# Kernel optimization log

Hardware: AMD Instinct MI355X
Metric: run time of the kernel (lower is better)

Reference implementation:

```python
import jax, jax.numpy as jnp
import numpy as np

N = 40000   # nodes
E = 600000  # edges
F = 128     # feature_size
H = 128     # hidden_channels
G = 32      # graphs in batch
C = 6       # classes


def setup_inputs() -> dict:
    key = jax.random.key(0)
    ks = jax.random.split(key, 20)
    x = jax.random.normal(ks[0], (N, F), jnp.float32)
    edge_index = jax.random.randint(ks[1], (2, E), 0, N, jnp.int32)
    batch = jnp.sort(jax.random.randint(ks[2], (N,), 0, G, jnp.int32))

    def lin_w(k, fan_in, fan_out):
        return jax.random.uniform(k, (fan_in, fan_out), jnp.float32,
                                  -1.0, 1.0) / np.sqrt(fan_in)

    inp = {"x": x, "edge_index": edge_index, "batch": batch,
           # GraphConv1: feature_size -> hidden (root + rel weights, bias)
           "w1_root": lin_w(ks[3], F, H), "w1_rel": lin_w(ks[4], F, H),
           "b1": jnp.zeros((H,), jnp.float32),
           # GraphConv2: hidden -> hidden
           "w2_root": lin_w(ks[5], H, H), "w2_rel": lin_w(ks[6], H, H),
           "b2": jnp.zeros((H,), jnp.float32),
           # GCNConv 3..5
           "w3": lin_w(ks[7], H, H), "b3": jnp.zeros((H,), jnp.float32),
           "w4": lin_w(ks[8], H, H), "b4": jnp.zeros((H,), jnp.float32),
           "w5": lin_w(ks[9], H, H), "b5": jnp.zeros((H,), jnp.float32),
           # final Linear(hidden, 6)
           "lin_w": lin_w(ks[10], H, C), "lin_b": jnp.zeros((C,), jnp.float32)}
    return inp


def _graph_conv(x, w_root, w_rel, b, src, dst, n):
    # PyG GraphConv (aggr='add'): out_i = W_root x_i + W_rel * sum_{j->i} x_j + b
    agg = jax.ops.segment_sum(x[src], dst, num_segments=n)
    return agg @ w_rel + x @ w_root + b


def _gcn_conv(x, w, b, src_sl, dst_sl, deg_inv_sqrt, n):
    # PyG GCNConv: out = D^-1/2 (A+I) D^-1/2 (X W) + b
    h = x @ w
    norm = deg_inv_sqrt[src_sl] * deg_inv_sqrt[dst_sl]  # [E+N]
    out = jax.ops.segment_sum(h[src_sl] * norm[:, None], dst_sl, num_segments=n)
    return out + b


def reference(x, edge_index, batch, w1_root, w1_rel, b1, w2_root, w2_rel, b2,
              w3, b3, w4, b4, w5, b5, lin_w, lin_b):
    src, dst = edge_index[0], edge_index[1]
    # self-loops for GCN layers
    loop = jnp.arange(N, dtype=edge_index.dtype)
    src_sl = jnp.concatenate([src, loop])
    dst_sl = jnp.concatenate([dst, loop])
    deg = jax.ops.segment_sum(jnp.ones((E + N,), x.dtype), dst_sl, num_segments=N)
    deg_inv_sqrt = jax.lax.rsqrt(deg)  # deg >= 1 due to self-loops

    h = jax.nn.relu(_graph_conv(x, w1_root, w1_rel, b1, src, dst, N))
    h = jax.nn.relu(_graph_conv(h, w2_root, w2_rel, b2, src, dst, N))
    h = jax.nn.relu(_gcn_conv(h, w3, b3, src_sl, dst_sl, deg_inv_sqrt, N))
    h = jax.nn.relu(_gcn_conv(h, w4, b4, src_sl, dst_sl, deg_inv_sqrt, N))
    h = _gcn_conv(h, w5, b5, src_sl, dst_sl, deg_inv_sqrt, N)

    # global_mean_pool over batch assignment
    counts = jax.ops.segment_sum(jnp.ones((N,), h.dtype), batch, num_segments=G)
    sums = jax.ops.segment_sum(h, batch, num_segments=G)
    embedding = sums / jnp.maximum(counts, 1.0)[:, None]  # [G, H]

    # dropout p=0.5 is identity in eval mode
    logits = embedding @ lin_w + lin_b  # [G, C]
    return (logits, embedding)
```

## Files before the change

kernel.cpp:

```cpp
#include <hip/hip_runtime.h>
#include <hip/hip_fp8.h>

#define Nn 40000
#define Ee 600000
#define Hh 128
#define Gg 32
#define Cc 6
#define CAP 64
#define NT (Nn / 16)
#define LSTR 136
#define PADW 0x9C409C40u

typedef __bf16 bf16x8 __attribute__((ext_vector_type(8)));
typedef float floatx4 __attribute__((ext_vector_type(4)));
typedef float floatx2 __attribute__((ext_vector_type(2)));
typedef unsigned short u16;
typedef unsigned int u32;
typedef unsigned char u8;

__device__ __forceinline__ u16 f2b(float f) {
    union { float f; u32 i; } v; v.f = f;
    u32 r = v.i + 0x7fffu + ((v.i >> 16) & 1u);
    return (u16)(r >> 16);
}
__device__ __forceinline__ u32 pack2(float a, float b) {
    return (u32)f2b(a) | ((u32)f2b(b) << 16);
}
__device__ __forceinline__ u8 f8e(float f) {
    __hip_fp8_e4m3 v(f); return (u8)v.__x;
}
__device__ __forceinline__ u8 f8e_hw(float f) {
    return (u8)(__builtin_amdgcn_cvt_pk_fp8_f32(f, f, 0, false) & 0xff);
}

__global__ __launch_bounds__(256) void k_setup(int* cursor, float* emb,
                                               u16* xb, u16* hA16, u8* xf8, u8* hA8, u8* hB8,
                                               float* dinv, u16* colidx,
                                               const float* __restrict__ x,
                                               const float* w0, const float* w1, const float* w2,
                                               const float* w3, const float* w4, const float* w5,
                                               const float* w6, u16* __restrict__ pwdst) {
    int gid = blockIdx.x * 256 + threadIdx.x;
    if (gid < Nn) cursor[gid] = 0;
    if (gid < Gg * Hh) emb[gid] = 0.f;
    if (blockIdx.x == 0) {
        int t = threadIdx.x;
        uint4 z = { 0, 0, 0, 0 };
        if (t < 16)              *(uint4*)(xb  + (size_t)Nn * 128 + t * 8) = z;
        else if (t < 32)         *(uint4*)(hA16 + (size_t)Nn * 128 + (t - 16) * 8) = z;
        else if (t < 40)         *(uint4*)(xf8 + (size_t)Nn * 128 + (t - 32) * 16) = z;
        else if (t < 48)         *(uint4*)(hA8 + (size_t)Nn * 128 + (t - 40) * 16) = z;
        else if (t < 56)         *(uint4*)(hB8 + (size_t)Nn * 128 + (t - 48) * 16) = z;
        else if (t == 56)        dinv[Nn] = 0.f;
    }
    if (blockIdx.x < 448) {
        int idx = gid;
        if (idx < 7 * 16384) {
            const float* ws[7] = { w0, w1, w2, w3, w4, w5, w6 };
            int mat = idx >> 14, r = idx & 16383;
            int j = r & 7, n = (r >> 3) & 15, q = (r >> 7) & 3, nt = (r >> 9) & 7, t = r >> 12;
            pwdst[idx] = f2b(ws[mat][(t * 32 + q * 8 + j) * 128 + nt * 16 + n]);
        }
    } else {
        int gid2 = (blockIdx.x - 448) * 256 + threadIdx.x;
        int i = gid2 * 4;
        float4 v = *(const float4*)(x + i);
        ushort4 o = { f2b(v.x), f2b(v.y), f2b(v.z), f2b(v.w) };
        *(ushort4*)(xb + i) = o;
        u32 p8 = (u32)f8e(v.x) | ((u32)f8e(v.y) << 8) | ((u32)f8e(v.z) << 16) | ((u32)f8e(v.w) << 24);
        *(u32*)(xf8 + i) = p8;
        *(u32*)(colidx + gid2 * 2) = PADW;
    }
}

__global__ __launch_bounds__(256) void k_scatter(const int* __restrict__ src, const int* __restrict__ dst,
                                                 int* __restrict__ cursor, u16* __restrict__ colidx) {
    int i = blockIdx.x * 256 + threadIdx.x;
    if (i < Ee) {
        int d = dst[i];
        int p = atomicAdd(&cursor[d], 1);
        if (p < CAP) colidx[d * CAP + p] = (u16)src[i];
    }
}

#define UPC_ADD(V) { floatx2 p_;                                                          \
    p_ = __builtin_amdgcn_cvt_pk_f32_fp8((int)(V).x, false); a0 += p_.x; a1 += p_.y;      \
    p_ = __builtin_amdgcn_cvt_pk_f32_fp8((int)(V).x, true);  a2 += p_.x; a3 += p_.y;      \
    p_ = __builtin_amdgcn_cvt_pk_f32_fp8((int)(V).y, false); a4 += p_.x; a5 += p_.y;      \
    p_ = __builtin_amdgcn_cvt_pk_f32_fp8((int)(V).y, true);  a6 += p_.x; a7 += p_.y; }

#define UPC_FMA(V, d) { floatx2 p_;                                                                 \
    p_ = __builtin_amdgcn_cvt_pk_f32_fp8((int)(V).x, false); a0 += (d) * p_.x; a1 += (d) * p_.y;    \
    p_ = __builtin_amdgcn_cvt_pk_f32_fp8((int)(V).x, true);  a2 += (d) * p_.x; a3 += (d) * p_.y;    \
    p_ = __builtin_amdgcn_cvt_pk_f32_fp8((int)(V).y, false); a4 += (d) * p_.x; a5 += (d) * p_.y;    \
    p_ = __builtin_amdgcn_cvt_pk_f32_fp8((int)(V).y, true);  a6 += (d) * p_.x; a7 += (d) * p_.y; }

__global__ __launch_bounds__(256) void k_layer(const u8* __restrict__ hin8,
                                               const u16* __restrict__ hin16,
                                               const u16* __restrict__ Bp_agg,
                                               const u16* __restrict__ Bp_self,
                                               const float* __restrict__ bias,
                                               u16* __restrict__ hout16,
                                               u8* __restrict__ hout8,
                                               const int* __restrict__ cursor,
                                               const u16* __restrict__ pcol,
                                               float* __restrict__ dinv,
                                               const int* __restrict__ batch,
                                               float* __restrict__ emb,
                                               int gcn, int relu, int dopool, int wrdinv) {
    __shared__ u16 Asm[16 * LSTR];
    __shared__ float Psm[16][132];
    int wave = threadIdx.x >> 6, lane = threadIdx.x & 63;
    int m0 = blockIdx.x * 16;

    {
        int g = lane >> 4, l = lane & 15;
        int nloc = wave * 4 + g;
        int node = m0 + nloc;
        int c = cursor[node]; if (c > CAP) c = CAP;
        if (wrdinv && l == 0) dinv[node] = rsqrtf((float)(c + 1));
        int beg = node * CAP;
        int end = beg + ((c + 7) & ~7);
        float a0 = 0.f, a1 = 0.f, a2 = 0.f, a3 = 0.f, a4 = 0.f, a5 = 0.f, a6 = 0.f, a7 = 0.f;
        const u8* b8 = hin8 + l * 8;
        if (beg < end) {
            uint4 ip = *(const uint4*)(pcol + beg);
            if (gcn) {
                for (int e = beg; e < end; e += 8) {
                    int en = (e + 8 < end) ? (e + 8) : beg;
                    uint4 jp = *(const uint4*)(pcol + en);
                    u32 e0 = ip.x & 0xFFFFu, e1 = ip.x >> 16;
                    u32 e2 = ip.y & 0xFFFFu, e3 = ip.y >> 16;
                    u32 e4 = ip.z & 0xFFFFu, e5 = ip.z >> 16;
                    u32 e6 = ip.w & 0xFFFFu, e7 = ip.w >> 16;
                    float d0 = dinv[e0], d1 = dinv[e1], d2 = dinv[e2], d3 = dinv[e3];
                    float d4 = dinv[e4], d5 = dinv[e5], d6 = dinv[e6], d7 = dinv[e7];
                    uint2 v0 = *(const uint2*)(b8 + (size_t)e0 * 128);
                    uint2 v1 = *(const uint2*)(b8 + (size_t)e1 * 128);
                    uint2 v2 = *(const uint2*)(b8 + (size_t)e2 * 128);
                    uint2 v3 = *(const uint2*)(b8 + (size_t)e3 * 128);
                    uint2 v4 = *(const uint2*)(b8 + (size_t)e4 * 128);
                    uint2 v5 = *(const uint2*)(b8 + (size_t)e5 * 128);
                    uint2 v6 = *(const uint2*)(b8 + (size_t)e6 * 128);
                    uint2 v7 = *(const uint2*)(b8 + (size_t)e7 * 128);
                    UPC_FMA(v0, d0) UPC_FMA(v1, d1) UPC_FMA(v2, d2) UPC_FMA(v3, d3)
                    UPC_FMA(v4, d4) UPC_FMA(v5, d5) UPC_FMA(v6, d6) UPC_FMA(v7, d7)
                    ip = jp;
                }
            } else {
                for (int e = beg; e < end; e += 8) {
                    int en = (e + 8 < end) ? (e + 8) : beg;
                    uint4 jp = *(const uint4*)(pcol + en);
                    u32 e0 = ip.x & 0xFFFFu, e1 = ip.x >> 16;
                    u32 e2 = ip.y & 0xFFFFu, e3 = ip.y >> 16;
                    u32 e4 = ip.z & 0xFFFFu, e5 = ip.z >> 16;
                    u32 e6 = ip.w & 0xFFFFu, e7 = ip.w >> 16;
                    uint2 v0 = *(const uint2*)(b8 + (size_t)e0 * 128);
                    uint2 v1 = *(const uint2*)(b8 + (size_t)e1 * 128);
                    uint2 v2 = *(const uint2*)(b8 + (size_t)e2 * 128);
                    uint2 v3 = *(const uint2*)(b8 + (size_t)e3 * 128);
                    uint2 v4 = *(const uint2*)(b8 + (size_t)e4 * 128);
                    uint2 v5 = *(const uint2*)(b8 + (size_t)e5 * 128);
                    uint2 v6 = *(const uint2*)(b8 + (size_t)e6 * 128);
                    uint2 v7 = *(const uint2*)(b8 + (size_t)e7 * 128);
                    UPC_ADD(v0) UPC_ADD(v1) UPC_ADD(v2) UPC_ADD(v3)
                    UPC_ADD(v4) UPC_ADD(v5) UPC_ADD(v6) UPC_ADD(v7)
                    ip = jp;
                }
            }
        }
        if (gcn) {
            float di = dinv[node], d2n = di * di;
            uint2 us = *(const uint2*)(b8 + (size_t)node * 128);
            a0 *= di; a1 *= di; a2 *= di; a3 *= di;
            a4 *= di; a5 *= di; a6 *= di; a7 *= di;
            UPC_FMA(us, d2n)
        }
        uint4 o = { pack2(a0, a1), pack2(a2, a3), pack2(a4, a5), pack2(a6, a7) };
        *(uint4*)&Asm[nloc * LSTR + l * 8] = o;
    }
    __syncthreads();

    {
        int n = lane & 15, q = lane >> 4;
        floatx4 acc0 = (floatx4){0.f, 0.f, 0.f, 0.f};
        floatx4 acc1 = (floatx4){0.f, 0.f, 0.f, 0.f};
        int nt0 = wave * 2, nt1 = wave * 2 + 1;
#pragma unroll
        for (int t = 0; t < 4; t++) {
            bf16x8 a = *(const bf16x8*)&Asm[n * LSTR + q * 8 + t * 32];
            const u16* bp = Bp_agg + t * 4096 + q * 128 + n * 8;
            bf16x8 b0 = *(const bf16x8*)(bp + nt0 * 512);
            bf16x8 b1 = *(const bf16x8*)(bp + nt1 * 512);
            acc0 = __builtin_amdgcn_mfma_f32_16x16x32_bf16(a, b0, acc0, 0, 0, 0);
            acc1 = __builtin_amdgcn_mfma_f32_16x16x32_bf16(a, b1, acc1, 0, 0, 0);
        }
        if (!gcn) {
            const u16* arow = hin16 + (size_t)(m0 + n) * 128 + q * 8;
#pragma unroll
            for (int t = 0; t < 4; t++) {
                bf16x8 a = *(const bf16x8*)(arow + t * 32);
                const u16* bp = Bp_self + t * 4096 + q * 128 + n * 8;
                bf16x8 b0 = *(const bf16x8*)(bp + nt0 * 512);
                bf16x8 b1 = *(const bf16x8*)(bp + nt1 * 512);
                acc0 = __builtin_amdgcn_mfma_f32_16x16x32_bf16(a, b0, acc0, 0, 0, 0);
                acc1 = __builtin_amdgcn_mfma_f32_16x16x32_bf16(a, b1, acc1, 0, 0, 0);
            }
        }
        if (dopool) {
#pragma unroll
            for (int j = 0; j < 2; j++) {
                int col = (wave * 2 + j) * 16 + n;
                float bv = bias[col];
                floatx4 ac = j ? acc1 : acc0;
#pragma unroll
                for (int r = 0; r < 4; r++)
                    Psm[q * 4 + r][col] = ac[r] + bv;
            }
            __syncthreads();
            if (threadIdx.x < 128) {
                int col = threadIdx.x;
                int g0 = batch[m0], g1 = batch[m0 + 15];
                for (int g = g0; g <= g1; ++g) {
                    float s = 0.f;
#pragma unroll
                    for (int i = 0; i < 16; ++i)
                        if (batch[m0 + i] == g) s += Psm[i][col];
                    atomicAdd(&emb[g * 128 + col], s);
                }
            }
        } else {
#pragma unroll
            for (int j = 0; j < 2; j++) {
                int col = (wave * 2 + j) * 16 + n;
                float bv = bias[col];
                floatx4 ac = j ? acc1 : acc0;
#pragma unroll
                for (int r = 0; r < 4; r++) {
                    float v = ac[r] + bv;
                    if (relu) v = fmaxf(v, 0.f);
                    size_t idx = (size_t)(m0 + q * 4 + r) * 128 + col;
                    if (hout16) hout16[idx] = f2b(v);
                    if (hout8)  hout8[idx]  = f8e_hw(v);
                }
            }
        }
    }
}

__global__ __launch_bounds__(256) void k_final(const float* __restrict__ emb, const int* __restrict__ batch,
                                               const float* __restrict__ lw, const float* __restrict__ lb,
                                               float* __restrict__ out) {
    __shared__ float cnt[Gg];
    int t = threadIdx.x;
    if (t < Gg) {
        int lo = 0, hi = Nn;
        while (lo < hi) { int m = (lo + hi) >> 1; if (batch[m] < t) lo = m + 1; else hi = m; }
        int lb0 = lo;
        lo = 0; hi = Nn;
        int tg = t + 1;
        while (lo < hi) { int m = (lo + hi) >> 1; if (batch[m] < tg) lo = m + 1; else hi = m; }
        cnt[t] = fmaxf((float)(lo - lb0), 1.f);
    }
    __syncthreads();
    for (int i = t; i < Gg * Hh; i += 256) {
        int g = i >> 7;
        out[Gg * Cc + i] = emb[i] / cnt[g];
    }
    if (t < Gg * Cc) {
        int g = t / Cc, c = t % Cc;
        float cn = cnt[g];
        float s = lb[c];
        for (int f = 0; f < Hh; f++)
            s += (emb[g * 128 + f] / cn) * lw[f * Cc + c];
        out[t] = s;
    }
}

extern "C" void kernel_launch(void* const* d_in, const int* in_sizes, int n_in,
                              void* d_out, int out_size, void* d_ws, size_t ws_size,
                              hipStream_t stream) {
    const float* x       = (const float*)d_in[0];
    const int*   ei      = (const int*)d_in[1];
    const int*   batch   = (const int*)d_in[2];
    const float* w1_root = (const float*)d_in[3];
    const float* w1_rel  = (const float*)d_in[4];
    const float* b1      = (const float*)d_in[5];
    const float* w2_root = (const float*)d_in[6];
    const float* w2_rel  = (const float*)d_in[7];
    const float* b2      = (const float*)d_in[8];
    const float* w3      = (const float*)d_in[9];
    const float* b3      = (const float*)d_in[10];
    const float* w4      = (const float*)d_in[11];
    const float* b4      = (const float*)d_in[12];
    const float* w5      = (const float*)d_in[13];
    const float* b5      = (const float*)d_in[14];
    const float* lw      = (const float*)d_in[15];
    const float* lb      = (const float*)d_in[16];
    const int* srcp = ei;
    const int* dstp = ei + Ee;
    float* out = (float*)d_out;

    char* w = (char*)d_ws;
    size_t off = 0;
    auto alloc = [&](size_t bytes) { size_t r = off; off += (bytes + 255) & ~(size_t)255; return r; };
    int*   cursor  = (int*)(w + alloc(Nn * 4));
    u16*   colidx  = (u16*)(w + alloc((size_t)Nn * CAP * 2));
    float* dinv    = (float*)(w + alloc((Nn + 1) * 4));
    float* emb     = (float*)(w + alloc(Gg * Hh * 4));
    u16*   pw      = (u16*)(w + alloc(7 * 16384 * 2));
    u16*   xb      = (u16*)(w + alloc((size_t)(Nn + 1) * Hh * 2));
    u16*   hA16    = (u16*)(w + alloc((size_t)(Nn + 1) * Hh * 2));
    u8*    xf8     = (u8*)(w + alloc((size_t)(Nn + 1) * Hh));
    u8*    hA8     = (u8*)(w + alloc((size_t)(Nn + 1) * Hh));
    u8*    hB8     = (u8*)(w + alloc((size_t)(Nn + 1) * Hh));
    (void)ws_size;

    u16* pw1r = pw + 0 * 16384;
    u16* pw1l = pw + 1 * 16384;
    u16* pw2r = pw + 2 * 16384;
    u16* pw2l = pw + 3 * 16384;
    u16* pw3  = pw + 4 * 16384;
    u16* pw4  = pw + 5 * 16384;
    u16* pw5  = pw + 6 * 16384;
    const u16* nil16 = (const u16*)nullptr;
    u16* no16 = (u16*)nullptr;
    u8*  no8  = (u8*)nullptr;

    hipLaunchKernelGGL(k_setup, dim3(448 + Nn * Hh / 1024), dim3(256), 0, stream,
                       cursor, emb, xb, hA16, xf8, hA8, hB8, dinv, colidx,
                       x, w1_root, w1_rel, w2_root, w2_rel, w3, w4, w5, pw);
    hipLaunchKernelGGL(k_scatter, dim3((Ee + 255) / 256), dim3(256), 0, stream,
                       srcp, dstp, cursor, colidx);

    hipLaunchKernelGGL(k_layer, dim3(NT), dim3(256), 0, stream,
                       xf8, xb, pw1l, pw1r, b1, hA16, hA8, cursor, colidx, dinv, batch, emb, 0, 1, 0, 1);
    hipLaunchKernelGGL(k_layer, dim3(NT), dim3(256), 0, stream,
                       hA8, hA16, pw2l, pw2r, b2, no16, hB8, cursor, colidx, dinv, batch, emb, 0, 1, 0, 0);
    hipLaunchKernelGGL(k_layer, dim3(NT), dim3(256), 0, stream,
                       hB8, nil16, pw3, nil16, b3, no16, hA8, cursor, colidx, dinv, batch, emb, 1, 1, 0, 0);
    hipLaunchKernelGGL(k_layer, dim3(NT), dim3(256), 0, stream,
                       hA8, nil16, pw4, nil16, b4, no16, xf8, cursor, colidx, dinv, batch, emb, 1, 1, 0, 0);
    hipLaunchKernelGGL(k_layer, dim3(NT), dim3(256), 0, stream,
                       xf8, nil16, pw5, nil16, b5, no16, no8, cursor, colidx, dinv, batch, emb, 1, 0, 1, 0);

    hipLaunchKernelGGL(k_final, dim3(1), dim3(256), 0, stream, emb, batch, lw, lb, out);
}
```

Baseline: 252.7 us.

## Bin edges by destination range before scattering into CSR adjacency

Replaces the single random scatter of edges into per-node adjacency lists with two passes. The first pass buckets packed (src,dst) pairs into 16 destination-range bins using shared-memory counters. The second pass scatters each bin, with block classes mapped to bin subsets so the atomics and colidx writes of concurrent blocks stay within a narrower, more cache-local address range. This costs an extra kernel launch and an extra write and read of the edge buffer, and it relies on the 16-bit packing of src and dst indices.

```diff
diff --git a/kernel.cpp b/kernel.cpp
--- a/kernel.cpp
+++ b/kernel.cpp
@@ -10,6 +10,8 @@
 #define NT (Nn / 16)
 #define LSTR 136
 #define PADW 0x9C409C40u
+#define NBIN 16
+#define BINCAP 40960
 
 typedef __bf16 bf16x8 __attribute__((ext_vector_type(8)));
 typedef float floatx4 __attribute__((ext_vector_type(4)));
@@ -33,7 +35,7 @@
     return (u8)(__builtin_amdgcn_cvt_pk_fp8_f32(f, f, 0, false) & 0xff);
 }
 
-__global__ __launch_bounds__(256) void k_setup(int* cursor, float* emb,
+__global__ __launch_bounds__(256) void k_setup(int* cursor, float* emb, int* gbin,
                                                u16* xb, u16* hA16, u8* xf8, u8* hA8, u8* hB8,
                                                float* dinv, u16* colidx,
                                                const float* __restrict__ x,
@@ -43,6 +45,7 @@
     int gid = blockIdx.x * 256 + threadIdx.x;
     if (gid < Nn) cursor[gid] = 0;
     if (gid < Gg * Hh) emb[gid] = 0.f;
+    if (gid < NBIN) gbin[gid] = 0;
     if (blockIdx.x == 0) {
         int t = threadIdx.x;
         uint4 z = { 0, 0, 0, 0 };
@@ -73,13 +76,50 @@
     }
 }
 
-__global__ __launch_bounds__(256) void k_scatter(const int* __restrict__ src, const int* __restrict__ dst,
-                                                 int* __restrict__ cursor, u16* __restrict__ colidx) {
-    int i = blockIdx.x * 256 + threadIdx.x;
+__global__ __launch_bounds__(256) void k_bin(const int* __restrict__ src, const int* __restrict__ dst,
+                                             int* __restrict__ gbin, u32* __restrict__ ebuf,
+                                             int* __restrict__ cursor, u16* __restrict__ colidx) {
+    __shared__ int cnt[NBIN];
+    __shared__ int base[NBIN];
+    int tid = threadIdx.x;
+    int i = blockIdx.x * 256 + tid;
+    if (tid < NBIN) cnt[tid] = 0;
+    __syncthreads();
+    int bin = -1, myslot = 0, s = 0, d = 0;
     if (i < Ee) {
-        int d = dst[i];
-        int p = atomicAdd(&cursor[d], 1);
-        if (p < CAP) colidx[d * CAP + p] = (u16)src[i];
+        s = src[i];
+        d = dst[i];
+        bin = d / 2500;
+        myslot = atomicAdd(&cnt[bin], 1);
+    }
+    __syncthreads();
+    if (tid < NBIN) base[tid] = (cnt[tid] > 0) ? atomicAdd(&gbin[tid], cnt[tid]) : 0;
+    __syncthreads();
+    if (bin >= 0) {
+        int slot = base[bin] + myslot;
+        if (slot < BINCAP) {
+            ebuf[bin * BINCAP + slot] = (u32)s | ((u32)d << 16);
+        } else {
+            int p = atomicAdd(&cursor[d], 1);
+            if (p < CAP) colidx[d * CAP + p] = (u16)s;
+        }
+    }
+}
+
+__global__ __launch_bounds__(256) void k_scatter2(const u32* __restrict__ ebuf, const int* __restrict__ gbin,
+                                                  int* __restrict__ cursor, u16* __restrict__ colidx) {
+    int cls = blockIdx.x & 7;
+    int idx = blockIdx.x >> 3;
+    int nidx = gridDim.x >> 3;
+    for (int b = cls; b < NBIN; b += 8) {
+        int n = gbin[b]; if (n > BINCAP) n = BINCAP;
+        const u32* eb = ebuf + b * BINCAP;
+        for (int e = idx * 256 + threadIdx.x; e < n; e += nidx * 256) {
+            u32 p = eb[e];
+            int d = p >> 16, s = p & 0xFFFFu;
+            int pos = atomicAdd(&cursor[d], 1);
+            if (pos < CAP) colidx[d * CAP + pos] = (u16)s;
+        }
     }
 }
 
@@ -306,6 +346,8 @@
     auto alloc = [&](size_t bytes) { size_t r = off; off += (bytes + 255) & ~(size_t)255; return r; };
     int*   cursor  = (int*)(w + alloc(Nn * 4));
     u16*   colidx  = (u16*)(w + alloc((size_t)Nn * CAP * 2));
+    u32*   ebuf    = (u32*)(w + alloc((size_t)NBIN * BINCAP * 4));
+    int*   gbin    = (int*)(w + alloc(256));
     float* dinv    = (float*)(w + alloc((Nn + 1) * 4));
     float* emb     = (float*)(w + alloc(Gg * Hh * 4));
     u16*   pw      = (u16*)(w + alloc(7 * 16384 * 2));
@@ -328,10 +370,12 @@
     u8*  no8  = (u8*)nullptr;
 
     hipLaunchKernelGGL(k_setup, dim3(448 + Nn * Hh / 1024), dim3(256), 0, stream,
-                       cursor, emb, xb, hA16, xf8, hA8, hB8, dinv, colidx,
+                       cursor, emb, gbin, xb, hA16, xf8, hA8, hB8, dinv, colidx,
                        x, w1_root, w1_rel, w2_root, w2_rel, w3, w4, w5, pw);
-    hipLaunchKernelGGL(k_scatter, dim3((Ee + 255) / 256), dim3(256), 0, stream,
-                       srcp, dstp, cursor, colidx);
+    hipLaunchKernelGGL(k_bin, dim3((Ee + 255) / 256), dim3(256), 0, stream,
+                       srcp, dstp, gbin, ebuf, cursor, colidx);
+    hipLaunchKernelGGL(k_scatter2, dim3(2048), dim3(256), 0, stream,
+                       ebuf, gbin, cursor, colidx);
 
     hipLaunchKernelGGL(k_layer, dim3(NT), dim3(256), 0, stream,
                        xf8, xb, pw1l, pw1r, b1, hA16, hA8, cursor, colidx, dinv, batch, emb, 0, 1, 0, 1);
```

Result: slower. 282.3 us (+11.7%).
